# Performance work log

Measured on AMD Instinct MI355X. Metric: run time of the kernel, lower is better.

The kernel has to match this reference:

```python
import jax, jax.numpy as jnp
import numpy as np

N, D = 100000, 64        # num nodes, node feature dim
E, DE = 1600000, 64      # num edges, edge feature dim
MSG_H, MSG_OUT = 128, 64 # message MLP hidden sizes (activate_final=True)
NODE_H = 128             # node MLP hidden; final size = D (residual)
LN_EPS = 1e-5


def setup_inputs() -> dict:
    key = jax.random.key(0)
    ks = jax.random.split(key, 10)
    def glorot(k, shape):
        fan_in = shape[0]
        return jax.random.normal(k, shape, jnp.float32) / jnp.sqrt(jnp.float32(fan_in))
    return {
        "nodes": jax.random.normal(ks[0], (N, D), jnp.float32),
        "edges": jax.random.normal(ks[1], (E, DE), jnp.float32),
        "senders": jax.random.randint(ks[2], (E,), 0, N, jnp.int32),
        "receivers": jax.random.randint(ks[3], (E,), 0, N, jnp.int32),
        "msg_W1": glorot(ks[4], (2 * D + DE, MSG_H)),
        "msg_b1": jnp.zeros((MSG_H,), jnp.float32),
        "msg_W2": glorot(ks[5], (MSG_H, MSG_OUT)),
        "msg_b2": jnp.zeros((MSG_OUT,), jnp.float32),
        "node_W1": glorot(ks[6], (D + MSG_OUT, NODE_H)),
        "node_b1": jnp.zeros((NODE_H,), jnp.float32),
        "node_W2": glorot(ks[7], (NODE_H, D)),
        "node_b2": jnp.zeros((D,), jnp.float32),
        "ln_scale": jnp.ones((D,), jnp.float32),
        "ln_offset": jnp.zeros((D,), jnp.float32),
    }


def reference(nodes, edges, senders, receivers,
              msg_W1, msg_b1, msg_W2, msg_b2,
              node_W1, node_b1, node_W2, node_b2,
              ln_scale, ln_offset):
    # --- message MLP (activate_final=True) over concat(sender, receiver, edge)
    x = jnp.concatenate([nodes[senders], nodes[receivers], edges], axis=-1)  # [E, 2D+DE]
    h = jax.nn.relu(x @ msg_W1 + msg_b1)
    messages = jax.nn.relu(h @ msg_W2 + msg_b2)  # [E, MSG_OUT]
    # --- aggregate messages at receivers
    agg = jax.ops.segment_sum(messages, receivers, num_segments=nodes.shape[0])  # [N, MSG_OUT]
    # --- node update MLP (no final activation), sizes [NODE_H, D] due to residual
    y = jnp.concatenate([nodes, agg], axis=-1)  # [N, D+MSG_OUT]
    y = jax.nn.relu(y @ node_W1 + node_b1)
    y = y @ node_W2 + node_b2  # [N, D]
    # --- layer norm over last axis with scale + offset
    mean = jnp.mean(y, axis=-1, keepdims=True)
    var = jnp.var(y, axis=-1, keepdims=True)
    y = (y - mean) * jax.lax.rsqrt(var + LN_EPS) * ln_scale + ln_offset
    # --- residual connection
    return nodes + y
```

## Files before the change

### kernel.cpp

```cpp
#include <hip/hip_runtime.h>

typedef short bf16x8 __attribute__((ext_vector_type(8)));
typedef float floatx4 __attribute__((ext_vector_type(4)));
typedef unsigned short u16x4 __attribute__((ext_vector_type(4)));
typedef unsigned short u16x8 __attribute__((ext_vector_type(8)));

__device__ __forceinline__ unsigned short f2bf(float f) {
  union { float f; unsigned int u; } v;
  v.f = f;
  unsigned int u = v.u + (0x7FFFu + ((v.u >> 16) & 1u));
  return (unsigned short)(u >> 16);
}

__device__ __forceinline__ bf16x8 pack8(float4 a, float4 b) {
  u16x8 h;
  h[0] = f2bf(a.x); h[1] = f2bf(a.y); h[2] = f2bf(a.z); h[3] = f2bf(a.w);
  h[4] = f2bf(b.x); h[5] = f2bf(b.y); h[6] = f2bf(b.z); h[7] = f2bf(b.w);
  union { u16x8 u; bf16x8 s; } cv; cv.u = h; return cv.s;
}

__global__ __launch_bounds__(256) void prep_weights(
    const float* __restrict__ mW1, const float* __restrict__ mW2,
    const float* __restrict__ nW1, const float* __restrict__ nW2,
    unsigned short* __restrict__ W1f, unsigned short* __restrict__ W2f,
    unsigned short* __restrict__ NW1f, unsigned short* __restrict__ NW2f) {
  int idx = blockIdx.x * 256 + threadIdx.x;
  if (idx < 24576) {
    int j = idx & 7, n = (idx >> 3) & 127, g = idx >> 10;
    W1f[idx] = f2bf(mW1[(g * 8 + j) * 128 + n]);
  } else if (idx < 32768) {
    int t = idx - 24576;
    int j = t & 7, n = (t >> 3) & 63, g = t >> 9;
    W2f[t] = f2bf(mW2[(g * 8 + j) * 64 + n]);
  } else if (idx < 49152) {
    int t = idx - 32768;
    int j = t & 7, n = (t >> 3) & 127, g = t >> 10;
    NW1f[t] = f2bf(nW1[(g * 8 + j) * 128 + n]);
  } else if (idx < 57344) {
    int t = idx - 49152;
    int j = t & 7, n = (t >> 3) & 63, g = t >> 9;
    NW2f[t] = f2bf(nW2[(g * 8 + j) * 64 + n]);
  }
}

__global__ __launch_bounds__(256) void conv_nodes(
    const float* __restrict__ nodes, unsigned short* __restrict__ nodes_bf, int total4) {
  int i = (blockIdx.x * 256 + threadIdx.x) * 4;
  if (i < total4) {
    float4 v = *(const float4*)(nodes + i);
    u16x4 h; h[0] = f2bf(v.x); h[1] = f2bf(v.y); h[2] = f2bf(v.z); h[3] = f2bf(v.w);
    *(u16x4*)(nodes_bf + i) = h;
  }
}

__global__ __launch_bounds__(256, 3) void edge_kernel(
    const float* __restrict__ edges, const unsigned short* __restrict__ nodes_bf,
    const int* __restrict__ senders, const int* __restrict__ receivers,
    const unsigned short* __restrict__ W1f, const unsigned short* __restrict__ W2f,
    const float* __restrict__ b1, const float* __restrict__ b2,
    float* agg, int E) {
  __shared__ unsigned short Hl[128 * 136];

  const int tid = threadIdx.x;
  const int e0 = blockIdx.x * 128;
  const int w = tid >> 6, lane = tid & 63;
  const int col = lane & 15, quad = lane >> 4;
  const int wm = w & 1, wn = w >> 1;

  int srow[4], sndi[4], rcvi[4];
#pragma unroll
  for (int mt = 0; mt < 4; ++mt) {
    int r = e0 + wm * 64 + mt * 16 + col;
    srow[mt] = r < E ? r : E - 1;
  }
#pragma unroll
  for (int mt = 0; mt < 4; ++mt) { sndi[mt] = senders[srow[mt]]; rcvi[mt] = receivers[srow[mt]]; }

  floatx4 z4 = {0.f, 0.f, 0.f, 0.f};
  floatx4 acc1[4][4];
#pragma unroll
  for (int mt = 0; mt < 4; ++mt)
#pragma unroll
    for (int nt = 0; nt < 4; ++nt) acc1[mt][nt] = z4;

#pragma unroll
  for (int ks = 0; ks < 4; ++ks) {
    bf16x8 a[4], b[4];
#pragma unroll
    for (int mt = 0; mt < 4; ++mt) {
      int nd = (ks < 2) ? sndi[mt] : rcvi[mt];
      a[mt] = *(const bf16x8*)&nodes_bf[(size_t)nd * 64 + (ks & 1) * 32 + quad * 8];
    }
#pragma unroll
    for (int nt = 0; nt < 4; ++nt)
      b[nt] = *(const bf16x8*)&W1f[ks * 4096 + quad * 1024 + (wn * 64 + nt * 16 + col) * 8];
#pragma unroll
    for (int mt = 0; mt < 4; ++mt)
#pragma unroll
      for (int nt = 0; nt < 4; ++nt)
        acc1[mt][nt] = __builtin_amdgcn_mfma_f32_16x16x32_bf16(a[mt], b[nt], acc1[mt][nt], 0, 0, 0);
  }
#pragma unroll
  for (int ks = 4; ks < 6; ++ks) {
    bf16x8 a[4], b[4];
#pragma unroll
    for (int mt = 0; mt < 4; ++mt) {
      const float* p = edges + (size_t)srow[mt] * 64 + (ks - 4) * 32 + quad * 8;
      float4 v0 = *(const float4*)p;
      float4 v1 = *(const float4*)(p + 4);
      a[mt] = pack8(v0, v1);
    }
#pragma unroll
    for (int nt = 0; nt < 4; ++nt)
      b[nt] = *(const bf16x8*)&W1f[ks * 4096 + quad * 1024 + (wn * 64 + nt * 16 + col) * 8];
#pragma unroll
    for (int mt = 0; mt < 4; ++mt)
#pragma unroll
      for (int nt = 0; nt < 4; ++nt)
        acc1[mt][nt] = __builtin_amdgcn_mfma_f32_16x16x32_bf16(a[mt], b[nt], acc1[mt][nt], 0, 0, 0);
  }

#pragma unroll
  for (int nt = 0; nt < 4; ++nt) {
    float bias = b1[wn * 64 + nt * 16 + col];
#pragma unroll
    for (int mt = 0; mt < 4; ++mt)
#pragma unroll
      for (int r = 0; r < 4; ++r) {
        float v = acc1[mt][nt][r] + bias;
        v = v > 0.f ? v : 0.f;
        Hl[(wm * 64 + mt * 16 + quad * 4 + r) * 136 + wn * 64 + nt * 16 + col] = f2bf(v);
      }
  }
  __syncthreads();

  floatx4 acc2[4][2];
#pragma unroll
  for (int mt = 0; mt < 4; ++mt) { acc2[mt][0] = z4; acc2[mt][1] = z4; }

#pragma unroll
  for (int ks = 0; ks < 4; ++ks) {
    bf16x8 a[4], b[2];
#pragma unroll
    for (int mt = 0; mt < 4; ++mt)
      a[mt] = *(const bf16x8*)&Hl[(wm * 64 + mt * 16 + col) * 136 + ks * 32 + quad * 8];
#pragma unroll
    for (int nt = 0; nt < 2; ++nt)
      b[nt] = *(const bf16x8*)&W2f[ks * 2048 + quad * 512 + (wn * 32 + nt * 16 + col) * 8];
#pragma unroll
    for (int mt = 0; mt < 4; ++mt)
#pragma unroll
      for (int nt = 0; nt < 2; ++nt)
        acc2[mt][nt] = __builtin_amdgcn_mfma_f32_16x16x32_bf16(a[mt], b[nt], acc2[mt][nt], 0, 0, 0);
  }

  float bs0 = b2[wn * 32 + col];
  float bs1 = b2[wn * 32 + 16 + col];
#pragma unroll
  for (int mt = 0; mt < 4; ++mt)
#pragma unroll
    for (int r = 0; r < 4; ++r) {
      int er = e0 + wm * 64 + mt * 16 + quad * 4 + r;
      if (er < E) {
        int rv = receivers[er];
        float v0 = acc2[mt][0][r] + bs0; v0 = v0 > 0.f ? v0 : 0.f;
        float v1 = acc2[mt][1][r] + bs1; v1 = v1 > 0.f ? v1 : 0.f;
        atomicAdd(&agg[(size_t)rv * 64 + wn * 32 + col], v0);
        atomicAdd(&agg[(size_t)rv * 64 + wn * 32 + 16 + col], v1);
      }
    }
}

__global__ __launch_bounds__(256, 3) void node_kernel(
    const float* __restrict__ nodes, const unsigned short* __restrict__ nodes_bf,
    const float* agg,
    const unsigned short* __restrict__ W1f, const unsigned short* __restrict__ W2f,
    const float* __restrict__ b1, const float* __restrict__ b2,
    const float* __restrict__ ln_s, const float* __restrict__ ln_o,
    float* out, int N) {
  __shared__ unsigned short Hl[128 * 136];
  __shared__ float Ls1[128][2];
  __shared__ float Ls2[128][2];

  const int tid = threadIdx.x;
  const int n0 = blockIdx.x * 128;
  const int w = tid >> 6, lane = tid & 63;
  const int col = lane & 15, quad = lane >> 4;
  const int wm = w & 1, wn = w >> 1;

  int arow[4];
#pragma unroll
  for (int mt = 0; mt < 4; ++mt) {
    int r = n0 + wm * 64 + mt * 16 + col;
    arow[mt] = r < N ? r : N - 1;
  }

  floatx4 z4 = {0.f, 0.f, 0.f, 0.f};
  floatx4 acc1[4][4];
#pragma unroll
  for (int mt = 0; mt < 4; ++mt)
#pragma unroll
    for (int nt = 0; nt < 4; ++nt) acc1[mt][nt] = z4;

#pragma unroll
  for (int ks = 0; ks < 2; ++ks) {
    bf16x8 a[4], b[4];
#pragma unroll
    for (int mt = 0; mt < 4; ++mt)
      a[mt] = *(const bf16x8*)&nodes_bf[(size_t)arow[mt] * 64 + ks * 32 + quad * 8];
#pragma unroll
    for (int nt = 0; nt < 4; ++nt)
      b[nt] = *(const bf16x8*)&W1f[ks * 4096 + quad * 1024 + (wn * 64 + nt * 16 + col) * 8];
#pragma unroll
    for (int mt = 0; mt < 4; ++mt)
#pragma unroll
      for (int nt = 0; nt < 4; ++nt)
        acc1[mt][nt] = __builtin_amdgcn_mfma_f32_16x16x32_bf16(a[mt], b[nt], acc1[mt][nt], 0, 0, 0);
  }
#pragma unroll
  for (int ks = 2; ks < 4; ++ks) {
    bf16x8 a[4], b[4];
#pragma unroll
    for (int mt = 0; mt < 4; ++mt) {
      const float* p = agg + (size_t)arow[mt] * 64 + (ks - 2) * 32 + quad * 8;
      float4 v0 = *(const float4*)p;
      float4 v1 = *(const float4*)(p + 4);
      a[mt] = pack8(v0, v1);
    }
#pragma unroll
    for (int nt = 0; nt < 4; ++nt)
      b[nt] = *(const bf16x8*)&W1f[ks * 4096 + quad * 1024 + (wn * 64 + nt * 16 + col) * 8];
#pragma unroll
    for (int mt = 0; mt < 4; ++mt)
#pragma unroll
      for (int nt = 0; nt < 4; ++nt)
        acc1[mt][nt] = __builtin_amdgcn_mfma_f32_16x16x32_bf16(a[mt], b[nt], acc1[mt][nt], 0, 0, 0);
  }

#pragma unroll
  for (int nt = 0; nt < 4; ++nt) {
    float bias = b1[wn * 64 + nt * 16 + col];
#pragma unroll
    for (int mt = 0; mt < 4; ++mt)
#pragma unroll
      for (int r = 0; r < 4; ++r) {
        float v = acc1[mt][nt][r] + bias;
        v = v > 0.f ? v : 0.f;
        Hl[(wm * 64 + mt * 16 + quad * 4 + r) * 136 + wn * 64 + nt * 16 + col] = f2bf(v);
      }
  }
  __syncthreads();

  floatx4 acc2[4][2];
#pragma unroll
  for (int mt = 0; mt < 4; ++mt) { acc2[mt][0] = z4; acc2[mt][1] = z4; }

#pragma unroll
  for (int ks = 0; ks < 4; ++ks) {
    bf16x8 a[4], b[2];
#pragma unroll
    for (int mt = 0; mt < 4; ++mt)
      a[mt] = *(const bf16x8*)&Hl[(wm * 64 + mt * 16 + col) * 136 + ks * 32 + quad * 8];
#pragma unroll
    for (int nt = 0; nt < 2; ++nt)
      b[nt] = *(const bf16x8*)&W2f[ks * 2048 + quad * 512 + (wn * 32 + nt * 16 + col) * 8];
#pragma unroll
    for (int mt = 0; mt < 4; ++mt)
#pragma unroll
      for (int nt = 0; nt < 2; ++nt)
        acc2[mt][nt] = __builtin_amdgcn_mfma_f32_16x16x32_bf16(a[mt], b[nt], acc2[mt][nt], 0, 0, 0);
  }

  float y[4][2][4];
  float bs0 = b2[wn * 32 + col];
  float bs1 = b2[wn * 32 + 16 + col];
#pragma unroll
  for (int mt = 0; mt < 4; ++mt)
#pragma unroll
    for (int r = 0; r < 4; ++r) {
      y[mt][0][r] = acc2[mt][0][r] + bs0;
      y[mt][1][r] = acc2[mt][1][r] + bs1;
    }

#pragma unroll
  for (int mt = 0; mt < 4; ++mt)
#pragma unroll
    for (int r = 0; r < 4; ++r) {
      float p1 = y[mt][0][r] + y[mt][1][r];
      float p2 = y[mt][0][r] * y[mt][0][r] + y[mt][1][r] * y[mt][1][r];
#pragma unroll
      for (int m = 1; m <= 8; m <<= 1) {
        p1 += __shfl_xor(p1, m);
        p2 += __shfl_xor(p2, m);
      }
      if (col == 0) {
        int row = wm * 64 + mt * 16 + quad * 4 + r;
        Ls1[row][wn] = p1;
        Ls2[row][wn] = p2;
      }
    }
  __syncthreads();

  float lsv0 = ln_s[wn * 32 + col], lsv1 = ln_s[wn * 32 + 16 + col];
  float lov0 = ln_o[wn * 32 + col], lov1 = ln_o[wn * 32 + 16 + col];
#pragma unroll
  for (int mt = 0; mt < 4; ++mt)
#pragma unroll
    for (int r = 0; r < 4; ++r) {
      int row = wm * 64 + mt * 16 + quad * 4 + r;
      int gi = n0 + row;
      float s1 = Ls1[row][0] + Ls1[row][1];
      float s2 = Ls2[row][0] + Ls2[row][1];
      float mean = s1 * (1.f / 64.f);
      float var = s2 * (1.f / 64.f) - mean * mean;
      float rstd = rsqrtf(var + 1e-5f);
      if (gi < N) {
        int j0 = wn * 32 + col;
        float o0 = (y[mt][0][r] - mean) * rstd * lsv0 + lov0 + nodes[(size_t)gi * 64 + j0];
        float o1 = (y[mt][1][r] - mean) * rstd * lsv1 + lov1 + nodes[(size_t)gi * 64 + j0 + 16];
        out[(size_t)gi * 64 + j0] = o0;
        out[(size_t)gi * 64 + j0 + 16] = o1;
      }
    }
}

extern "C" void kernel_launch(void* const* d_in, const int* in_sizes, int n_in,
                              void* d_out, int out_size, void* d_ws, size_t ws_size,
                              hipStream_t stream) {
  const float* nodes     = (const float*)d_in[0];
  const float* edges     = (const float*)d_in[1];
  const int*   senders   = (const int*)d_in[2];
  const int*   receivers = (const int*)d_in[3];
  const float* msg_W1    = (const float*)d_in[4];
  const float* msg_b1    = (const float*)d_in[5];
  const float* msg_W2    = (const float*)d_in[6];
  const float* msg_b2    = (const float*)d_in[7];
  const float* node_W1   = (const float*)d_in[8];
  const float* node_b1   = (const float*)d_in[9];
  const float* node_W2   = (const float*)d_in[10];
  const float* node_b2   = (const float*)d_in[11];
  const float* ln_scale  = (const float*)d_in[12];
  const float* ln_offset = (const float*)d_in[13];

  const int N = in_sizes[0] / 64;
  const int E = in_sizes[2];

  unsigned short* W1f  = (unsigned short*)d_ws;
  unsigned short* W2f  = W1f + 24576;
  unsigned short* NW1f = W2f + 8192;
  unsigned short* NW2f = NW1f + 16384;
  unsigned short* nodes_bf = NW2f + 8192;

  float* agg = (float*)d_out;

  hipMemsetAsync(d_out, 0, (size_t)out_size * sizeof(float), stream);
  prep_weights<<<224, 256, 0, stream>>>(msg_W1, msg_W2, node_W1, node_W2, W1f, W2f, NW1f, NW2f);
  conv_nodes<<<(N * 64 + 1023) / 1024, 256, 0, stream>>>(nodes, nodes_bf, N * 64);
  edge_kernel<<<(E + 127) / 128, 256, 0, stream>>>(edges, nodes_bf, senders, receivers,
                                                   W1f, W2f, msg_b1, msg_b2, agg, E);
  node_kernel<<<(N + 127) / 128, 256, 0, stream>>>(nodes, nodes_bf, agg, NW1f, NW2f,
                                                   node_b1, node_b2, ln_scale, ln_offset,
                                                   (float*)d_out, N);
}
```

Before: 1.011 ms.

## Replace atomic scatter-add with CSR sort by receiver and segmented gather-sum

Builds a CSR index of edges grouped by receiver (count, three-stage scan, scatter), runs the edge MLP in sorted order writing bf16 messages to a buffer, and has the node kernel sum each node's contiguous message rows before the node MLP. The goal is to remove the 100M float atomicAdds into agg. In exchange it adds several preprocessing kernels, random gathers of edge features through s_eid, a 200MB bf16 message write and read, and bf16 rounding of the messages and their sum.

```diff
diff --git a/kernel.cpp b/kernel.cpp
--- a/kernel.cpp
+++ b/kernel.cpp
@@ -11,7 +11,9 @@
   unsigned int u = v.u + (0x7FFFu + ((v.u >> 16) & 1u));
   return (unsigned short)(u >> 16);
 }
-
+__device__ __forceinline__ float bf2f(unsigned short h) {
+  union { unsigned int u; float f; } v; v.u = ((unsigned int)h) << 16; return v.f;
+}
 __device__ __forceinline__ bf16x8 pack8(float4 a, float4 b) {
   u16x8 h;
   h[0] = f2bf(a.x); h[1] = f2bf(a.y); h[2] = f2bf(a.z); h[3] = f2bf(a.w);
@@ -53,28 +55,91 @@
   }
 }
 
+__global__ __launch_bounds__(256) void k_count(
+    const int* __restrict__ rcv, int* __restrict__ cnt, int E) {
+  int e = blockIdx.x * 256 + threadIdx.x;
+  if (e < E) atomicAdd(&cnt[rcv[e]], 1);
+}
+
+__global__ __launch_bounds__(256) void k_scan1(
+    const int* __restrict__ cnt, int* __restrict__ rowptr, int* __restrict__ aux, int N) {
+  __shared__ int wsum[4];
+  int tid = threadIdx.x, lane = tid & 63, wid = tid >> 6;
+  int i = blockIdx.x * 256 + tid;
+  int v = (i < N) ? cnt[i] : 0;
+  int x = v;
+#pragma unroll
+  for (int d = 1; d < 64; d <<= 1) {
+    int t = __shfl_up(x, d);
+    if (lane >= d) x += t;
+  }
+  if (lane == 63) wsum[wid] = x;
+  __syncthreads();
+  int off = 0;
+#pragma unroll
+  for (int k = 0; k < 4; ++k) if (k < wid) off += wsum[k];
+  if (i < N) rowptr[i] = off + x - v;
+  if (tid == 0) aux[blockIdx.x] = wsum[0] + wsum[1] + wsum[2] + wsum[3];
+}
+
+__global__ __launch_bounds__(512) void k_scan2(int* __restrict__ aux, int NB) {
+  __shared__ int s[512];
+  int t = threadIdx.x;
+  int orig = (t < NB) ? aux[t] : 0;
+  s[t] = orig;
+  __syncthreads();
+  for (int d = 1; d < 512; d <<= 1) {
+    int v = (t >= d) ? s[t - d] : 0;
+    __syncthreads();
+    s[t] += v;
+    __syncthreads();
+  }
+  if (t < NB) aux[t] = s[t] - orig;
+}
+
+__global__ __launch_bounds__(256) void k_scan3(
+    int* __restrict__ rowptr, const int* __restrict__ aux, int N, int E) {
+  int i = blockIdx.x * 256 + threadIdx.x;
+  if (i < N) rowptr[i] += aux[i >> 8];
+  if (i == 0) rowptr[N] = E;
+}
+
+__global__ __launch_bounds__(256) void k_scatter(
+    const int* __restrict__ snd, const int* __restrict__ rcv,
+    const int* __restrict__ rowptr, int* __restrict__ cur,
+    int* __restrict__ s_snd, int* __restrict__ s_rcv, int* __restrict__ s_eid, int E) {
+  int e = blockIdx.x * 256 + threadIdx.x;
+  if (e < E) {
+    int r = rcv[e];
+    int pos = rowptr[r] + atomicAdd(&cur[r], 1);
+    s_snd[pos] = snd[e];
+    s_rcv[pos] = r;
+    s_eid[pos] = e;
+  }
+}
+
 __global__ __launch_bounds__(256, 3) void edge_kernel(
     const float* __restrict__ edges, const unsigned short* __restrict__ nodes_bf,
-    const int* __restrict__ senders, const int* __restrict__ receivers,
+    const int* __restrict__ s_snd, const int* __restrict__ s_rcv,
+    const int* __restrict__ s_eid,
     const unsigned short* __restrict__ W1f, const unsigned short* __restrict__ W2f,
     const float* __restrict__ b1, const float* __restrict__ b2,
-    float* agg, int E) {
-  __shared__ unsigned short Hl[128 * 136];
+    unsigned short* __restrict__ msg, int E) {
+  __shared__ __align__(16) unsigned short Hl[128 * 136];
 
   const int tid = threadIdx.x;
-  const int e0 = blockIdx.x * 128;
+  const int p0 = blockIdx.x * 128;
   const int w = tid >> 6, lane = tid & 63;
   const int col = lane & 15, quad = lane >> 4;
   const int wm = w & 1, wn = w >> 1;
 
-  int srow[4], sndi[4], rcvi[4];
+  int sndi[4], rcvi[4], eidi[4];
 #pragma unroll
   for (int mt = 0; mt < 4; ++mt) {
-    int r = e0 + wm * 64 + mt * 16 + col;
-    srow[mt] = r < E ? r : E - 1;
-  }
-#pragma unroll
-  for (int mt = 0; mt < 4; ++mt) { sndi[mt] = senders[srow[mt]]; rcvi[mt] = receivers[srow[mt]]; }
+    int p = p0 + wm * 64 + mt * 16 + col;
+    p = p < E ? p : E - 1;
+    sndi[mt] = s_snd[p]; rcvi[mt] = s_rcv[p]; eidi[mt] = s_eid[p];
+  }
 
   floatx4 z4 = {0.f, 0.f, 0.f, 0.f};
   floatx4 acc1[4][4];
@@ -105,7 +170,7 @@
     bf16x8 a[4], b[4];
 #pragma unroll
     for (int mt = 0; mt < 4; ++mt) {
-      const float* p = edges + (size_t)srow[mt] * 64 + (ks - 4) * 32 + quad * 8;
+      const float* p = edges + (size_t)eidi[mt] * 64 + (ks - 4) * 32 + quad * 8;
       float4 v0 = *(const float4*)p;
       float4 v1 = *(const float4*)(p + 4);
       a[mt] = pack8(v0, v1);
@@ -153,6 +218,7 @@
       for (int nt = 0; nt < 2; ++nt)
         acc2[mt][nt] = __builtin_amdgcn_mfma_f32_16x16x32_bf16(a[mt], b[nt], acc2[mt][nt], 0, 0, 0);
   }
+  __syncthreads();
 
   float bs0 = b2[wn * 32 + col];
   float bs1 = b2[wn * 32 + 16 + col];
@@ -160,25 +226,33 @@
   for (int mt = 0; mt < 4; ++mt)
 #pragma unroll
     for (int r = 0; r < 4; ++r) {
-      int er = e0 + wm * 64 + mt * 16 + quad * 4 + r;
-      if (er < E) {
-        int rv = receivers[er];
-        float v0 = acc2[mt][0][r] + bs0; v0 = v0 > 0.f ? v0 : 0.f;
-        float v1 = acc2[mt][1][r] + bs1; v1 = v1 > 0.f ? v1 : 0.f;
-        atomicAdd(&agg[(size_t)rv * 64 + wn * 32 + col], v0);
-        atomicAdd(&agg[(size_t)rv * 64 + wn * 32 + 16 + col], v1);
-      }
-    }
+      int row = wm * 64 + mt * 16 + quad * 4 + r;
+      float v0 = acc2[mt][0][r] + bs0; v0 = v0 > 0.f ? v0 : 0.f;
+      float v1 = acc2[mt][1][r] + bs1; v1 = v1 > 0.f ? v1 : 0.f;
+      Hl[row * 72 + wn * 32 + col] = f2bf(v0);
+      Hl[row * 72 + wn * 32 + 16 + col] = f2bf(v1);
+    }
+  __syncthreads();
+
+  {
+    int row = tid >> 1, c0 = (tid & 1) * 32;
+    if (p0 + row < E) {
+#pragma unroll
+      for (int k = 0; k < 4; ++k)
+        *(u16x8*)&msg[(size_t)(p0 + row) * 64 + c0 + k * 8] =
+            *(const u16x8*)&Hl[row * 72 + c0 + k * 8];
+    }
+  }
 }
 
 __global__ __launch_bounds__(256, 3) void node_kernel(
     const float* __restrict__ nodes, const unsigned short* __restrict__ nodes_bf,
-    const float* agg,
+    const unsigned short* __restrict__ msg, const int* __restrict__ rowptr,
     const unsigned short* __restrict__ W1f, const unsigned short* __restrict__ W2f,
     const float* __restrict__ b1, const float* __restrict__ b2,
     const float* __restrict__ ln_s, const float* __restrict__ ln_o,
-    float* out, int N) {
-  __shared__ unsigned short Hl[128 * 136];
+    float* __restrict__ out, int N) {
+  __shared__ __align__(16) unsigned short Hl[128 * 136];
   __shared__ float Ls1[128][2];
   __shared__ float Ls2[128][2];
 
@@ -188,6 +262,26 @@
   const int col = lane & 15, quad = lane >> 4;
   const int wm = w & 1, wn = w >> 1;
 
+  for (int k = 0; k < 32; ++k) {
+    int nl = w * 32 + k;
+    int n = n0 + nl;
+    float acc = 0.f;
+    if (n < N) {
+      int s = rowptr[n], e = rowptr[n + 1];
+      int i = s;
+      for (; i + 4 <= e; i += 4) {
+        float a0 = bf2f(msg[(size_t)(i + 0) * 64 + lane]);
+        float a1 = bf2f(msg[(size_t)(i + 1) * 64 + lane]);
+        float a2 = bf2f(msg[(size_t)(i + 2) * 64 + lane]);
+        float a3 = bf2f(msg[(size_t)(i + 3) * 64 + lane]);
+        acc += (a0 + a1) + (a2 + a3);
+      }
+      for (; i < e; ++i) acc += bf2f(msg[(size_t)i * 64 + lane]);
+    }
+    Hl[nl * 72 + lane] = f2bf(acc);
+  }
+  __syncthreads();
+
   int arow[4];
 #pragma unroll
   for (int mt = 0; mt < 4; ++mt) {
@@ -221,12 +315,8 @@
   for (int ks = 2; ks < 4; ++ks) {
     bf16x8 a[4], b[4];
 #pragma unroll
-    for (int mt = 0; mt < 4; ++mt) {
-      const float* p = agg + (size_t)arow[mt] * 64 + (ks - 2) * 32 + quad * 8;
-      float4 v0 = *(const float4*)p;
-      float4 v1 = *(const float4*)(p + 4);
-      a[mt] = pack8(v0, v1);
-    }
+    for (int mt = 0; mt < 4; ++mt)
+      a[mt] = *(const bf16x8*)&Hl[(wm * 64 + mt * 16 + col) * 72 + (ks - 2) * 32 + quad * 8];
 #pragma unroll
     for (int nt = 0; nt < 4; ++nt)
       b[nt] = *(const bf16x8*)&W1f[ks * 4096 + quad * 1024 + (wn * 64 + nt * 16 + col) * 8];
@@ -236,6 +326,7 @@
       for (int nt = 0; nt < 4; ++nt)
         acc1[mt][nt] = __builtin_amdgcn_mfma_f32_16x16x32_bf16(a[mt], b[nt], acc1[mt][nt], 0, 0, 0);
   }
+  __syncthreads();
 
 #pragma unroll
   for (int nt = 0; nt < 4; ++nt) {
@@ -344,21 +435,44 @@
 
   const int N = in_sizes[0] / 64;
   const int E = in_sizes[2];
-
-  unsigned short* W1f  = (unsigned short*)d_ws;
-  unsigned short* W2f  = W1f + 24576;
-  unsigned short* NW1f = W2f + 8192;
-  unsigned short* NW2f = NW1f + 16384;
-  unsigned short* nodes_bf = NW2f + 8192;
-
-  float* agg = (float*)d_out;
-
-  hipMemsetAsync(d_out, 0, (size_t)out_size * sizeof(float), stream);
+  const int NB = (N + 255) / 256;
+
+  char* p = (char*)d_ws;
+  auto take = [&](size_t bytes) {
+    char* q = p;
+    p += (bytes + 255) & ~(size_t)255;
+    return q;
+  };
+  unsigned short* W1f      = (unsigned short*)take(24576 * 2);
+  unsigned short* W2f      = (unsigned short*)take(8192 * 2);
+  unsigned short* NW1f     = (unsigned short*)take(16384 * 2);
+  unsigned short* NW2f     = (unsigned short*)take(8192 * 2);
+  unsigned short* nodes_bf = (unsigned short*)take((size_t)N * 64 * 2);
+  int* cnt      = (int*)take((size_t)NB * 256 * 4);
+  int* cur      = (int*)take((size_t)NB * 256 * 4);
+  int* rowptr   = (int*)take(((size_t)N + 1) * 4);
+  int* aux      = (int*)take((size_t)NB * 4);
+  int* s_snd    = (int*)take((size_t)E * 4);
+  int* s_rcv    = (int*)take((size_t)E * 4);
+  int* s_eid    = (int*)take((size_t)E * 4);
+  unsigned short* msg = (unsigned short*)take((size_t)E * 64 * 2);
+
+  hipMemsetAsync(cnt, 0, (size_t)NB * 256 * 4, stream);
+  hipMemsetAsync(cur, 0, (size_t)NB * 256 * 4, stream);
+
   prep_weights<<<224, 256, 0, stream>>>(msg_W1, msg_W2, node_W1, node_W2, W1f, W2f, NW1f, NW2f);
   conv_nodes<<<(N * 64 + 1023) / 1024, 256, 0, stream>>>(nodes, nodes_bf, N * 64);
-  edge_kernel<<<(E + 127) / 128, 256, 0, stream>>>(edges, nodes_bf, senders, receivers,
-                                                   W1f, W2f, msg_b1, msg_b2, agg, E);
-  node_kernel<<<(N + 127) / 128, 256, 0, stream>>>(nodes, nodes_bf, agg, NW1f, NW2f,
-                                                   node_b1, node_b2, ln_scale, ln_offset,
-                                                   (float*)d_out, N);
-}
+
+  k_count<<<(E + 255) / 256, 256, 0, stream>>>(receivers, cnt, E);
+  k_scan1<<<NB, 256, 0, stream>>>(cnt, rowptr, aux, N);
+  k_scan2<<<1, 512, 0, stream>>>(aux, NB);
+  k_scan3<<<NB, 256, 0, stream>>>(rowptr, aux, N, E);
+  k_scatter<<<(E + 255) / 256, 256, 0, stream>>>(senders, receivers, rowptr, cur,
+                                                 s_snd, s_rcv, s_eid, E);
+
+  edge_kernel<<<(E + 127) / 128, 256, 0, stream>>>(edges, nodes_bf, s_snd, s_rcv, s_eid,
+                                                   W1f, W2f, msg_b1, msg_b2, msg, E);
+  node_kernel<<<(N + 127) / 128, 256, 0, stream>>>(nodes, nodes_bf, msg, rowptr,
+                                                   NW1f, NW2f, node_b1, node_b2,
+                                                   ln_scale, ln_offset, (float*)d_out, N);
+}
```

Result: slower. 1.107 ms (+9.6%).
